# Kernel tuning notes

Measured on AMD Instinct MI355X. Metric: run time of the kernel, lower is better.

## Reference

```python
import jax, jax.numpy as jnp
import numpy as np

L = 3          # atom_decoder_depth
HEADS = 8      # spatial attention heads
T_HEADS = 8    # temporal attention heads
WQ = 32        # atoms_per_window_queries
HK = 128       # atoms_per_window_keys
EPS = 1e-5


def _ln(x, g=None, b=None):
    mu = jnp.mean(x, -1, keepdims=True)
    v = jnp.mean((x - mu) ** 2, -1, keepdims=True)
    xn = (x - mu) * jax.lax.rsqrt(v + EPS)
    if g is not None:
        xn = xn * g + b
    return xn


def _adaln(a, s, w_sc, b_sc, w_sk):
    # adaptive LN: sigmoid-scaled normed activations + conditioned skip
    sn = _ln(s)
    return jax.nn.sigmoid(sn @ w_sc + b_sc) * _ln(a) + sn @ w_sk


def setup_inputs() -> dict:
    key = jax.random.key(0)
    ks = iter(jax.random.split(key, 64))
    B0, T, N, M, D, TS = 1, 8, 1024, 4096, 256, 768
    HID = 2 * D

    def rn(shape, s=1.0):
        return jax.random.normal(next(ks), shape, jnp.float32) * s

    NW = (M + WQ - 1) // WQ
    a = rn((B0 * T, N, 2 * TS))
    q = rn((B0 * T, M, D))
    c = rn((B0 * T, M, D))
    atom_dec_bias = rn((B0, NW, WQ, HK, L * HEADS), 0.1)
    tok_idx = jnp.sort(jax.random.randint(next(ks), (B0, M), 0, N), axis=-1)
    atom_to_token = jax.nn.one_hot(tok_idx, N, dtype=jnp.float32)
    atom_pad_mask = jnp.ones((B0, M), bool)
    timestamps = jnp.sort(jax.random.uniform(next(ks), (B0, T)) * 10.0, axis=-1)
    p = 0.02
    return dict(
        a=a, q=q, c=c, atom_dec_bias=atom_dec_bias,
        atom_to_token=atom_to_token, atom_pad_mask=atom_pad_mask,
        timestamps=timestamps,
        W_a2q=rn((2 * TS, D), p),
        ada1_sw=rn((L, D, D), p), ada1_sb=rn((L, D), p), ada1_kw=rn((L, D, D), p),
        attn_wq=rn((L, D, D), p), attn_bq=rn((L, D), p),
        attn_wk=rn((L, D, D), p), attn_wv=rn((L, D, D), p),
        attn_wg=rn((L, D, D), p), attn_wo=rn((L, D, D), p),
        og_w=rn((L, D, D), p), og_b=rn((L, D), p),
        ada2_sw=rn((L, D, D), p), ada2_sb=rn((L, D), p), ada2_kw=rn((L, D, D), p),
        tr_w1=rn((L, D, HID), p), tr_w2=rn((L, D, HID), p), tr_w3=rn((L, HID, D), p),
        tr_gw=rn((L, D, D), p), tr_gb=rn((L, D), p),
        t_ln_g=jnp.ones((L, D)), t_ln_b=jnp.zeros((L, D)),
        t_wq=rn((L, D, D), p), t_wk=rn((L, D, D), p), t_wv=rn((L, D, D), p),
        t_wg=rn((L, D, D), p), t_wo=rn((L, D, D), p),
        t_decay=rn((L, T_HEADS)),
        pos_g=jnp.ones((D,)), pos_b=jnp.zeros((D,)), pos_w=rn((D, 3), p),
        T=8,
    )


def _forward(a, q, c, atom_dec_bias, atom_to_token, atom_pad_mask, timestamps,
             W_a2q, ada1_sw, ada1_sb, ada1_kw, attn_wq, attn_bq, attn_wk,
             attn_wv, attn_wg, attn_wo, og_w, og_b, ada2_sw, ada2_sb, ada2_kw,
             tr_w1, tr_w2, tr_w3, tr_gw, tr_gb, t_ln_g, t_ln_b, t_wq, t_wk,
             t_wv, t_wg, t_wo, t_decay, pos_g, pos_b, pos_w, T):
    BT, N, _ = a.shape
    B0 = BT // T
    M0, D = q.shape[1], q.shape[2]
    NW = (M0 + WQ - 1) // WQ
    M = NW * WQ
    h, dh = HEADS, D // HEADS
    th, tdh = T_HEADS, D // T_HEADS

    # token -> atom gather via one-hot matmul (atom_to_token shared across T)
    a2q = jnp.einsum('bmn,btnd->btmd', atom_to_token,
                     (a @ W_a2q).reshape(B0, T, N, D)).reshape(BT, M0, D)
    q = q + a2q

    pad = M - M0
    qf = jnp.pad(q, ((0, 0), (0, pad), (0, 0)))
    cf = jnp.pad(c, ((0, 0), (0, pad), (0, 0)))
    mask = jnp.pad(atom_pad_mask, ((0, 0), (0, pad)))  # (B0, M)

    side = (HK - WQ) // 2
    # index map: query window w attends keys [w*WQ - side, w*WQ - side + HK)
    widx = jnp.arange(NW)[:, None] * WQ + jnp.arange(HK)[None, :]

    def window_keys(x):  # (B, M, D) -> (B, NW, HK, D)
        xp = jnp.pad(x, ((0, 0), (side, side), (0, 0)))
        return xp[:, widx]

    kmask = jnp.pad(mask, ((0, 0), (side, side)))[:, widx]  # (B0, NW, HK)
    neg = jnp.where(kmask[:, None, :, None, None, :], 0.0, -1e9)

    bias = atom_dec_bias.reshape(B0, NW, WQ, HK, L, HEADS)
    inv_s = 1.0 / np.sqrt(dh).astype(np.float32)
    inv_t = 1.0 / np.sqrt(tdh).astype(np.float32)
    dt = jnp.abs(timestamps[:, :, None] - timestamps[:, None, :])  # (B0,T,T)

    for i in range(L):
        # ---- spatial windowed attention with pair bias ----
        b = _adaln(qf, cf, ada1_sw[i], ada1_sb[i], ada1_kw[i])
        qh = (b @ attn_wq[i] + attn_bq[i]).reshape(BT, NW, WQ, h, dh)
        kin = window_keys(b)                                   # (BT,NW,HK,D)
        kh = (kin @ attn_wk[i]).reshape(BT, NW, HK, h, dh)
        vh = (kin @ attn_wv[i]).reshape(BT, NW, HK, h, dh)
        logits = jnp.einsum('bnqhd,bnkhd->bnhqk', qh, kh) * inv_s
        logits = logits.reshape(B0, T, NW, h, WQ, HK)
        logits = logits + bias[:, :, :, :, i].transpose(0, 1, 4, 2, 3)[:, None] + neg
        p_attn = jax.nn.softmax(logits, axis=-1).reshape(BT, NW, h, WQ, HK)
        o = jnp.einsum('bnhqk,bnkhd->bnqhd', p_attn, vh)
        g = jax.nn.sigmoid(b @ attn_wg[i]).reshape(BT, NW, WQ, h, dh)
        o = (g * o).reshape(BT, M, D) @ attn_wo[i]
        qf = qf + jax.nn.sigmoid(cf @ og_w[i] + og_b[i]) * o
        # conditioned SwiGLU transition
        t = _adaln(qf, cf, ada2_sw[i], ada2_sb[i], ada2_kw[i])
        x = jax.nn.silu(t @ tr_w1[i]) * (t @ tr_w2[i])
        qf = qf + jax.nn.sigmoid(cf @ tr_gw[i] + tr_gb[i]) * (x @ tr_w3[i])
        # ---- temporal attention with per-head decay bias ----
        xt = qf.reshape(B0, T, M, D).transpose(0, 2, 1, 3)     # (B0,M,T,D)
        xn = _ln(xt, t_ln_g[i], t_ln_b[i])
        tq = (xn @ t_wq[i]).reshape(B0, M, T, th, tdh)
        tk = (xn @ t_wk[i]).reshape(B0, M, T, th, tdh)
        tv = (xn @ t_wv[i]).reshape(B0, M, T, th, tdh)
        tl = jnp.einsum('bmqhd,bmkhd->bmhqk', tq, tk) * inv_t
        decay = jax.nn.softplus(t_decay[i])                    # (th,)
        tl = tl - decay[None, None, :, None, None] * dt[:, None, None]
        tp = jax.nn.softmax(tl, axis=-1)
        to = jnp.einsum('bmhqk,bmkhd->bmqhd', tp, tv).reshape(B0, M, T, D)
        tg = jax.nn.sigmoid(xn @ t_wg[i])
        xt = xt + (tg * to) @ t_wo[i]
        qf = xt.transpose(0, 2, 1, 3).reshape(BT, M, D)

    q_out = qf[:, :M0]
    return _ln(q_out, pos_g, pos_b) @ pos_w  # (B*T, M0, 3)


def reference(a, q, c, atom_dec_bias, atom_to_token, atom_pad_mask, timestamps,
              W_a2q, ada1_sw, ada1_sb, ada1_kw, attn_wq, attn_bq, attn_wk,
              attn_wv, attn_wg, attn_wo, og_w, og_b, ada2_sw, ada2_sb, ada2_kw,
              tr_w1, tr_w2, tr_w3, tr_gw, tr_gb, t_ln_g, t_ln_b, t_wq, t_wk,
              t_wv, t_wg, t_wo, t_decay, pos_g, pos_b, pos_w, T):
    return _forward(a, q, c, atom_dec_bias, atom_to_token, atom_pad_mask,
                    timestamps, W_a2q, ada1_sw, ada1_sb, ada1_kw, attn_wq,
                    attn_bq, attn_wk, attn_wv, attn_wg, attn_wo, og_w, og_b,
                    ada2_sw, ada2_sb, ada2_kw, tr_w1, tr_w2, tr_w3, tr_gw,
                    tr_gb, t_ln_g, t_ln_b, t_wq, t_wk, t_wv, t_wg, t_wo,
                    t_decay, pos_g, pos_b, pos_w, T)
```

## Files before the change

kernel.cpp:

```cpp
#include <hip/hip_runtime.h>
#include <cstddef>
#include <cstdint>

#define DEVI __device__ __forceinline__

typedef __attribute__((ext_vector_type(8))) __bf16 bf16x8;
typedef __attribute__((ext_vector_type(8))) unsigned short us8;
typedef __attribute__((ext_vector_type(4))) unsigned short us4;
typedef __attribute__((ext_vector_type(4))) float f32x4;

constexpr int B0_ = 1, T_ = 8, N_ = 1024, M_ = 4096, D_ = 256;
constexpr int BT_ = 8, NW_ = 128, WQ_ = 32, HK_ = 128, SIDE_ = 48;
constexpr int R_ = BT_ * M_;
constexpr size_t Fq = 8388608;

DEVI unsigned short f2b(float f) {
  return __builtin_bit_cast(unsigned short, static_cast<__bf16>(f));
}
DEVI float b2f(unsigned short s) { return __uint_as_float(((unsigned)s) << 16); }
DEVI float sigm(float x) { return 1.0f / (1.0f + __expf(-x)); }
DEVI bf16x8 ld_bf8(const unsigned short* p) {
  return __builtin_bit_cast(bf16x8, *(const us8*)p);
}
DEVI bf16x8 pack_f8(float4 v0, float4 v1) {
  bf16x8 r;
  r[0] = (__bf16)v0.x; r[1] = (__bf16)v0.y; r[2] = (__bf16)v0.z; r[3] = (__bf16)v0.w;
  r[4] = (__bf16)v1.x; r[5] = (__bf16)v1.y; r[6] = (__bf16)v1.z; r[7] = (__bf16)v1.w;
  return r;
}
DEVI void mfma_bf16(f32x4& c, bf16x8 a, bf16x8 b) {
  c = __builtin_amdgcn_mfma_f32_16x16x32_bf16(a, b, c, 0, 0, 0);
}
DEVI void gload16(const void* g, void* l) {
  __builtin_amdgcn_global_load_lds((__attribute__((address_space(1))) void*)g,
                                   (__attribute__((address_space(3))) void*)l, 16, 0, 0);
}

struct ConvArgs {
  const float* src[64];
  int doff[64];
  int Kd[64];
  int Nd[64];
  float scale[64];
  int n;
};

__global__ __launch_bounds__(256) void conv_k(ConvArgs ca, unsigned short* __restrict__ wbf) {
  int e = blockIdx.x;
  int K = ca.Kd[e], N = ca.Nd[e];
  int nx = N >> 6, nk = K >> 6;
  int t = blockIdx.y;
  if (t >= nx * nk) return;
  int tx = t % nx, tk = t / nx;
  const float* s = ca.src[e];
  float sc = ca.scale[e];
  unsigned short* d = wbf + ca.doff[e];
  int n = tx * 64 + (threadIdx.x & 63);
  int k0 = tk * 64 + (threadIdx.x >> 6) * 16;
  for (int r = 0; r < 16; r++) {
    int k = k0 + r;
    d[(size_t)n * K + k] = f2b(s[(size_t)k * N + n] * sc);
  }
}

__global__ __launch_bounds__(256) void cvt_k(const float* __restrict__ s,
                                             unsigned short* __restrict__ d, int n8) {
  int i = blockIdx.x * 256 + threadIdx.x;
  if (i >= n8) return;
  float4 v0 = *(const float4*)(s + (size_t)i * 8);
  float4 v1 = *(const float4*)(s + (size_t)i * 8 + 4);
  *(us8*)(d + (size_t)i * 8) = __builtin_bit_cast(us8, pack_f8(v0, v1));
}

__global__ __launch_bounds__(256) void bias_prep_k(
    const float* __restrict__ bq, const float* __restrict__ sb1,
    const float* __restrict__ sb2, const float* __restrict__ ogb,
    const float* __restrict__ trb, float* __restrict__ bias) {
  int t = threadIdx.x;
  const float inv_s = 0.17677669529663687f;
  for (int i = t; i < 1024 + 3 * 2560; i += 256) bias[i] = 0.f;
  __syncthreads();
  for (int i = 0; i < 3; i++) {
    float* B = bias + 1024 + i * 2560;
    B[t]        = bq[i * 256 + t] * inv_s;
    B[1024 + t] = sb1[i * 256 + t];
    B[1536 + t] = sb2[i * 256 + t];
    B[2048 + t] = ogb[i * 256 + t];
    B[2304 + t] = trb[i * 256 + t];
  }
}

__global__ __launch_bounds__(256) void biasb_k(const float* __restrict__ adb,
                                               unsigned short* __restrict__ biasb) {
  __shared__ float ld[3072];
  int rq = blockIdx.x;
  int t = threadIdx.x;
  const float* src = adb + (size_t)rq * 3072;
  for (int i = t; i < 3072; i += 256) ld[i] = src[i];
  __syncthreads();
  int k = t & 127;
  int pk = (k & 15) * 8 + (k >> 4);
  int ak = (rq >> 5) * 32 - SIDE_ + k;
  float maskv = ((unsigned)ak < (unsigned)M_) ? 0.f : -1e9f;
  for (int lh = t >> 7; lh < 24; lh += 2)
    biasb[((size_t)lh * 4096 + rq) * 128 + pk] = f2b(ld[k * 24 + lh] + maskv);
}

__global__ __launch_bounds__(256) void tokidx_k(const float* __restrict__ a2t,
                                                int* __restrict__ idx) {
  int m = blockIdx.x * 4 + (threadIdx.x >> 6);
  int lane = threadIdx.x & 63;
  int best = -1;
  for (int j = 0; j < 16; j++) {
    int col = lane * 16 + j;
    if (a2t[(size_t)m * 1024 + col] > 0.5f) best = col;
  }
#pragma unroll
  for (int off = 1; off < 64; off <<= 1) best = max(best, __shfl_xor(best, off));
  if (lane == 0) idx[m] = best;
}

__global__ __launch_bounds__(256) void qfinitln_k(const float* __restrict__ q,
                                                  const unsigned short* __restrict__ tokf,
                                                  const int* __restrict__ idx,
                                                  float* __restrict__ qf,
                                                  unsigned short* __restrict__ lnout) {
  int wid = threadIdx.x >> 6, lane = threadIdx.x & 63;
  size_t row = (size_t)blockIdx.x * 4 + wid;
  int m = (int)(row & 4095);
  int bt = (int)(row >> 12);
  float4 qv = *(const float4*)(q + row * 256 + lane * 4);
  us4 tv = *(const us4*)(tokf + ((size_t)bt * 1024 + idx[m]) * 256 + lane * 4);
  float x[4];
  x[0] = qv.x + b2f(tv[0]); x[1] = qv.y + b2f(tv[1]);
  x[2] = qv.z + b2f(tv[2]); x[3] = qv.w + b2f(tv[3]);
  *(float4*)(qf + row * 256 + lane * 4) = make_float4(x[0], x[1], x[2], x[3]);
  float s = x[0] + x[1] + x[2] + x[3];
  float sq = x[0] * x[0] + x[1] * x[1] + x[2] * x[2] + x[3] * x[3];
#pragma unroll
  for (int o = 1; o < 64; o <<= 1) {
    s += __shfl_xor(s, o);
    sq += __shfl_xor(sq, o);
  }
  float mu = s * 0.00390625f;
  float rs = rsqrtf(sq * 0.00390625f - mu * mu + 1e-5f);
  us4 r;
#pragma unroll
  for (int j = 0; j < 4; j++) r[j] = f2b((x[j] - mu) * rs);
  *(us4*)(lnout + row * 256 + lane * 4) = r;
}

__global__ __launch_bounds__(256) void ln_k(const float* __restrict__ src,
                                            unsigned short* __restrict__ dst) {
  size_t row = (size_t)blockIdx.x * 4 + (threadIdx.x >> 6);
  int lane = threadIdx.x & 63;
  float4 v = ((const float4*)(src + row * 256))[lane];
  float s = v.x + v.y + v.z + v.w;
#pragma unroll
  for (int o = 1; o < 64; o <<= 1) s += __shfl_xor(s, o);
  float mu = s * 0.00390625f;
  float dx = v.x - mu, dy = v.y - mu, dz = v.z - mu, dw = v.w - mu;
  float qv = dx * dx + dy * dy + dz * dz + dw * dw;
#pragma unroll
  for (int o = 1; o < 64; o <<= 1) qv += __shfl_xor(qv, o);
  float rs = rsqrtf(qv * 0.00390625f + 1e-5f);
  us4 r;
  r[0] = f2b(dx * rs); r[1] = f2b(dy * rs); r[2] = f2b(dz * rs); r[3] = f2b(dw * rs);
  *(us4*)(dst + row * 256 + lane * 4) = r;
}

template <int K, int EP, int PAIR>
__global__ __launch_bounds__(256) void gemm4_k(
    const unsigned short* __restrict__ A, const unsigned short* __restrict__ Wt,
    const float* __restrict__ bias, unsigned short* __restrict__ out,
    const unsigned short* __restrict__ lnq, unsigned short* __restrict__ vtb,
    int NOUT) {
  constexpr int NT = K / 64;
  __shared__ __align__(16) unsigned short S[2][16384];
  const int tid = threadIdx.x;
  const int lane = tid & 63, w = tid >> 6;
  const int lg = lane >> 4, lr = lane & 15;
  const int wr = w >> 1, wc = w & 1;
  const size_t m_base = (size_t)blockIdx.x * 128;
  const size_t n_base = (size_t)blockIdx.y * 64;
  const int srow = w * 8 + (lane >> 3);
  const int scol = ((lane & 7) ^ (lane >> 3)) * 8;
  const unsigned short* gA = A + (m_base + srow) * K + scol;
  const unsigned short* gB = Wt + (n_base + srow) * K + scol;
  const unsigned short* gB2 = Wt + (n_base + PAIR + srow) * K + scol;
  f32x4 acc[4][2] = {};
  f32x4 acc2[4][2] = {};
  const int swz = lr & 7;

  auto stage = [&](int buf, int t) {
    unsigned short* Sb = S[buf];
    const int kk = t * 64;
#pragma unroll
    for (int j = 0; j < 4; j++)
      gload16(gA + (size_t)(j * 32) * K + kk, Sb + w * 512 + j * 2048);
#pragma unroll
    for (int j = 0; j < 2; j++)
      gload16(gB + (size_t)(j * 32) * K + kk, Sb + 8192 + w * 512 + j * 2048);
#pragma unroll
    for (int j = 0; j < 2; j++)
      gload16(gB2 + (size_t)(j * 32) * K + kk, Sb + 12288 + w * 512 + j * 2048);
  };
  auto compute = [&](int buf) {
    const unsigned short* Sb = S[buf];
#pragma unroll
    for (int ks = 0; ks < 2; ks++) {
      const int co = ((ks * 4 + lg) ^ swz) << 3;
      bf16x8 af[4], b1[2], b2[2];
#pragma unroll
      for (int i = 0; i < 4; i++)
        af[i] = ld_bf8(Sb + (wr * 64 + i * 16 + lr) * 64 + co);
#pragma unroll
      for (int i = 0; i < 2; i++) {
        b1[i] = ld_bf8(Sb + 8192 + (wc * 32 + i * 16 + lr) * 64 + co);
        b2[i] = ld_bf8(Sb + 12288 + (wc * 32 + i * 16 + lr) * 64 + co);
      }
      __builtin_amdgcn_s_setprio(1);
#pragma unroll
      for (int mi = 0; mi < 4; mi++)
#pragma unroll
        for (int ni = 0; ni < 2; ni++) {
          mfma_bf16(acc[mi][ni], af[mi], b1[ni]);
          mfma_bf16(acc2[mi][ni], af[mi], b2[ni]);
        }
      __builtin_amdgcn_s_setprio(0);
    }
  };

  stage(0, 0);
  __syncthreads();
  int cur = 0;
  for (int t = 0; t < NT - 1; t++) {
    stage(cur ^ 1, t + 1);
    compute(cur);
    __syncthreads();
    cur ^= 1;
  }
  compute(cur);
  __syncthreads();

  unsigned short* St = S[0];
  auto emit_half = [&](int cbase, bool second) {
#pragma unroll
    for (int mi = 0; mi < 4; mi++)
#pragma unroll
      for (int ni = 0; ni < 2; ni++)
#pragma unroll
        for (int r = 0; r < 4; r++) {
          int rowl = wr * 64 + mi * 16 + lg * 4 + r;
          int cl = wc * 32 + ni * 16 + lr;
          float v = (second ? acc2[mi][ni][r] : acc[mi][ni][r]) + bias[cbase + cl];
          St[rowl * 64 + (((cl >> 3) ^ (rowl & 7)) << 3) + (cl & 7)] = f2b(v);
        }
    __syncthreads();
#pragma unroll
    for (int p = 0; p < 4; p++) {
      int rowl = p * 32 + (tid >> 3);
      int chunk = tid & 7;
      us8 v = *(const us8*)(St + rowl * 64 + ((chunk ^ (rowl & 7)) << 3));
      *(us8*)(out + (m_base + rowl) * NOUT + cbase + chunk * 8) = v;
    }
    __syncthreads();
  };

  if constexpr (EP == 1) {
    emit_half((int)n_base, false);
    emit_half((int)n_base + PAIR, true);
  } else if constexpr (EP == 6) {
    emit_half((int)n_base, false);
    if ((int)n_base < 256) {
      const int bt = (int)(m_base >> 12);
      const int m0 = (int)(m_base & 4095);
#pragma unroll
      for (int mi = 0; mi < 4; mi++)
#pragma unroll
        for (int ni = 0; ni < 2; ni++) {
          int cl = wc * 32 + ni * 16 + lr;
          int rowb = wr * 64 + mi * 16 + lg * 4;
          us4 val;
#pragma unroll
          for (int r = 0; r < 4; r++)
            val[r] = f2b(acc2[mi][ni][r] + bias[(int)n_base + cl + 512]);
          *(us4*)(St + cl * 128 + (((rowb >> 3) ^ (cl & 7)) << 3) + (rowb & 7)) = val;
        }
      __syncthreads();
#pragma unroll
      for (int p = 0; p < 4; p++) {
        int cl = tid >> 2;
        int rc = (tid & 3) + p * 4;
        us8 v = *(const us8*)(St + cl * 128 + ((rc ^ (cl & 7)) << 3));
        *(us8*)(vtb + ((size_t)bt * 256 + n_base + cl) * 4096 + m0 + rc * 8) = v;
      }
    } else {
      emit_half((int)n_base + 512, true);
    }
  } else {
#pragma unroll
    for (int mi = 0; mi < 4; mi++)
#pragma unroll
      for (int ni = 0; ni < 2; ni++)
#pragma unroll
        for (int r = 0; r < 4; r++) {
          int rowl = wr * 64 + mi * 16 + lg * 4 + r;
          int cl = wc * 32 + ni * 16 + lr;
          size_t grow = m_base + rowl;
          int gcol = (int)n_base + cl;
          float v = acc[mi][ni][r] + bias[gcol];
          float v2 = acc2[mi][ni][r] + bias[gcol + PAIR];
          unsigned short res;
          if constexpr (EP == 4) {
            res = f2b(sigm(v) * b2f(lnq[grow * 256 + gcol]) + v2);
          } else {
            res = f2b(v * sigm(v) * v2);
          }
          St[rowl * 64 + (((cl >> 3) ^ (rowl & 7)) << 3) + (cl & 7)] = res;
        }
    __syncthreads();
#pragma unroll
    for (int p = 0; p < 4; p++) {
      int rowl = p * 32 + (tid >> 3);
      int chunk = tid & 7;
      us8 v = *(const us8*)(St + rowl * 64 + ((chunk ^ (rowl & 7)) << 3));
      *(us8*)(out + (m_base + rowl) * NOUT + n_base + chunk * 8) = v;
    }
  }
}

template <int K, bool GATED>
__global__ __launch_bounds__(512) void gemmln_k(
    const unsigned short* __restrict__ A, const unsigned short* __restrict__ Wt,
    float* __restrict__ qf, const unsigned short* __restrict__ gate, int goff,
    unsigned short* __restrict__ lnout, const float* __restrict__ lng,
    const float* __restrict__ lnb) {
  constexpr int NT = K / 64;
  __shared__ __align__(16) unsigned short S[2][20480];
  const int tid = threadIdx.x;
  const int lane = tid & 63, w = tid >> 6;
  const int lg = lane >> 4, lr = lane & 15;
  const size_t m_base = (size_t)blockIdx.x * 64;
  const int srow = lane >> 3;
  const int scol = ((lane & 7) ^ srow) * 8;
  const unsigned short* gA = A + (m_base + w * 8 + srow) * K + scol;
  const unsigned short* gB = Wt + (w * 32 + srow) * K + scol;
  f32x4 acc[4][2] = {};
  const int swz = lr & 7;

  auto stage = [&](int buf, int t) {
    unsigned short* Sb = S[buf];
    const int kk = t * 64;
    gload16(gA + kk, Sb + w * 512);
#pragma unroll
    for (int j = 0; j < 4; j++)
      gload16(gB + (size_t)(j * 8) * K + kk, Sb + 4096 + w * 2048 + j * 512);
  };
  auto compute = [&](int buf) {
    const unsigned short* Sb = S[buf];
#pragma unroll
    for (int ks = 0; ks < 2; ks++) {
      const int co = ((ks * 4 + lg) ^ swz) << 3;
      bf16x8 af[4], bf1[2];
#pragma unroll
      for (int i = 0; i < 4; i++) af[i] = ld_bf8(Sb + (i * 16 + lr) * 64 + co);
#pragma unroll
      for (int i = 0; i < 2; i++)
        bf1[i] = ld_bf8(Sb + 4096 + (w * 32 + i * 16 + lr) * 64 + co);
      __builtin_amdgcn_s_setprio(1);
#pragma unroll
      for (int mi = 0; mi < 4; mi++)
#pragma unroll
        for (int ni = 0; ni < 2; ni++) mfma_bf16(acc[mi][ni], af[mi], bf1[ni]);
      __builtin_amdgcn_s_setprio(0);
    }
  };

  stage(0, 0);
  __syncthreads();
  int cur = 0;
  for (int t = 0; t < NT - 1; t++) {
    stage(cur ^ 1, t + 1);
    compute(cur);
    __syncthreads();
    cur ^= 1;
  }
  compute(cur);
  __syncthreads();

  unsigned short* St = S[0];
#pragma unroll
  for (int mi = 0; mi < 4; mi++)
#pragma unroll
    for (int ni = 0; ni < 2; ni++)
#pragma unroll
      for (int r = 0; r < 4; r++) {
        int rowl = mi * 16 + lg * 4 + r;
        int col = w * 32 + ni * 16 + lr;
        size_t grow = m_base + rowl;
        float v = acc[mi][ni][r];
        if constexpr (GATED) v *= sigm(b2f(gate[grow * 512 + goff + col]));
        float nq = qf[grow * 256 + col] + v;
        qf[grow * 256 + col] = nq;
        St[rowl * 256 + (((col >> 3) ^ (rowl & 7)) << 3) + (col & 7)] = f2b(nq);
      }
  __syncthreads();
  float gv[4], bv[4];
  if (lng) {
#pragma unroll
    for (int j = 0; j < 4; j++) {
      gv[j] = lng[lane * 4 + j];
      bv[j] = lnb[lane * 4 + j];
    }
  }
  const int rchunk = lane >> 1;
  const int rsub = (lane & 1) << 2;
  for (int rr = 0; rr < 8; rr++) {
    int rowl = w * 8 + rr;
    us4 vv = *(const us4*)(St + rowl * 256 + ((rchunk ^ (rowl & 7)) << 3) + rsub);
    float x[4];
#pragma unroll
    for (int j = 0; j < 4; j++) x[j] = b2f(vv[j]);
    float s = x[0] + x[1] + x[2] + x[3];
    float sq = x[0] * x[0] + x[1] * x[1] + x[2] * x[2] + x[3] * x[3];
#pragma unroll
    for (int o = 1; o < 64; o <<= 1) {
      s += __shfl_xor(s, o);
      sq += __shfl_xor(sq, o);
    }
    float mu = s * 0.00390625f;
    float rs = rsqrtf(sq * 0.00390625f - mu * mu + 1e-5f);
    us4 r;
#pragma unroll
    for (int j = 0; j < 4; j++) {
      float y = (x[j] - mu) * rs;
      if (lng) y = y * gv[j] + bv[j];
      r[j] = f2b(y);
    }
    *(us4*)(lnout + (m_base + rowl) * 256 + lane * 4) = r;
  }
}

__global__ __launch_bounds__(256) void attn_k(const unsigned short* __restrict__ big1,
                                              const unsigned short* __restrict__ vtbuf,
                                              const unsigned short* __restrict__ biasb,
                                              unsigned short* __restrict__ o, int layer) {
  __shared__ __align__(16) unsigned short pl_s[4][32 * 128];
  const int bid = blockIdx.x;
  const int nid = (bid & 7) * 256 + (bid >> 3);
  const int w = nid & 127, bt = (nid >> 7) & 7, hg = nid >> 10;
  const int tid = threadIdx.x, wid = tid >> 6, lane = tid & 63;
  const int lg = lane >> 4, lr = lane & 15;
  const int h = hg * 4 + wid;
  unsigned short* pl = pl_s[wid];
  const size_t base = (size_t)bt * M_;

  bf16x8 aq[2];
#pragma unroll
  for (int mi = 0; mi < 2; mi++)
    aq[mi] = ld_bf8(big1 + (base + w * 32 + mi * 16 + lr) * 1024 + h * 32 + lg * 8);
  f32x4 lac[2][8] = {};
#pragma unroll
  for (int ni = 0; ni < 8; ni++) {
    int kidx = ni * 16 + lr;
    int ak = w * 32 - SIDE_ + kidx;
    int akc = ak < 0 ? 0 : (ak > M_ - 1 ? M_ - 1 : ak);
    bf16x8 bk = ld_bf8(big1 + (base + akc) * 1024 + 256 + h * 32 + lg * 8);
    __builtin_amdgcn_s_setprio(1);
    mfma_bf16(lac[0][ni], aq[0], bk);
    mfma_bf16(lac[1][ni], aq[1], bk);
    __builtin_amdgcn_s_setprio(0);
  }
  const unsigned short* bb0 =
      biasb + (((size_t)(layer * 8 + h)) * 4096 + w * 32) * 128 + lr * 8;
  float invs[2][4];
#pragma unroll
  for (int mi = 0; mi < 2; mi++)
#pragma unroll
    for (int r = 0; r < 4; r++) {
      int qrow = mi * 16 + lg * 4 + r;
      us8 bb = *(const us8*)(bb0 + (size_t)qrow * 128);
      float lv[8];
      float mx = -3e38f;
#pragma unroll
      for (int ni = 0; ni < 8; ni++) {
        float x = lac[mi][ni][r] + b2f(bb[ni]);
        lv[ni] = x;
        mx = fmaxf(mx, x);
      }
#pragma unroll
      for (int off = 1; off < 16; off <<= 1) mx = fmaxf(mx, __shfl_xor(mx, off));
      float sum = 0.f;
#pragma unroll
      for (int ni = 0; ni < 8; ni++) {
        float e = __expf(lv[ni] - mx);
        lv[ni] = e;
        sum += e;
      }
#pragma unroll
      for (int off = 1; off < 16; off <<= 1) sum += __shfl_xor(sum, off);
      invs[mi][r] = 1.f / sum;
      int sw = (qrow & 7) << 3;
#pragma unroll
      for (int ni = 0; ni < 8; ni++)
        pl[qrow * 128 + ((ni * 16 + lr) ^ sw)] = f2b(lv[ni]);
    }
  const unsigned short* vrow0 = vtbuf + ((size_t)bt * 256 + h * 32 + lr) * 4096;
  const unsigned short* vrow1 = vrow0 + (size_t)16 * 4096;
  f32x4 oc[2][2] = {};
#pragma unroll
  for (int ks = 0; ks < 4; ks++) {
    int kcol = w * 32 - SIDE_ + ks * 32 + lg * 8;
    kcol = kcol < 0 ? 0 : (kcol > M_ - 8 ? M_ - 8 : kcol);
    bf16x8 bv0 = ld_bf8(vrow0 + kcol);
    bf16x8 bv1 = ld_bf8(vrow1 + kcol);
    int kswz = (ks * 32 + lg * 8) ^ ((lr & 7) << 3);
    bf16x8 ap0 = ld_bf8(pl + lr * 128 + kswz);
    bf16x8 ap1 = ld_bf8(pl + (16 + lr) * 128 + kswz);
    __builtin_amdgcn_s_setprio(1);
    mfma_bf16(oc[0][0], ap0, bv0);
    mfma_bf16(oc[0][1], ap0, bv1);
    mfma_bf16(oc[1][0], ap1, bv0);
    mfma_bf16(oc[1][1], ap1, bv1);
    __builtin_amdgcn_s_setprio(0);
  }
#pragma unroll
  for (int mi = 0; mi < 2; mi++)
#pragma unroll
    for (int nd = 0; nd < 2; nd++)
#pragma unroll
      for (int r = 0; r < 4; r++) {
        int qrow = mi * 16 + lg * 4 + r;
        int d = nd * 16 + lr;
        size_t rowi = base + w * 32 + qrow;
        float gv = sigm(b2f(big1[rowi * 1024 + 768 + h * 32 + d]));
        o[rowi * 256 + h * 32 + d] = f2b(oc[mi][nd][r] * invs[mi][r] * gv);
      }
}

__global__ __launch_bounds__(256) void tattn_k(const unsigned short* __restrict__ big1,
                                               const float* __restrict__ ts,
                                               const float* __restrict__ tdec,
                                               unsigned short* __restrict__ o, int layer) {
  __shared__ __align__(16) unsigned short lds[4][8 * 768];
  int wid = threadIdx.x >> 6, lane = threadIdx.x & 63;
  int m = blockIdx.x * 4 + wid;
  unsigned short* Lp = lds[wid];
  for (int it = 0; it < 12; it++) {
    int u = it * 64 + lane;
    int t = u / 96, pos = (u % 96) * 8;
    *(uint4*)(Lp + t * 768 + pos) =
        *(const uint4*)(big1 + ((size_t)(t * M_ + m)) * 1024 + pos);
  }
  __syncthreads();
  int th = lane >> 3, qt = lane & 7;
  float decay = log1pf(__expf(tdec[layer * 8 + th]));
  float tsq = ts[qt];
  const float inv_t = 0.17677669529663687f;
  float tqv[32];
#pragma unroll
  for (int d = 0; d < 32; d++) tqv[d] = b2f(Lp[qt * 768 + th * 32 + d]);
  float lv[8];
  float mx = -3e38f;
#pragma unroll
  for (int kt = 0; kt < 8; kt++) {
    float dot = 0.f;
#pragma unroll
    for (int d = 0; d < 32; d++) dot += tqv[d] * b2f(Lp[kt * 768 + 256 + th * 32 + d]);
    float x = dot * inv_t - decay * fabsf(tsq - ts[kt]);
    lv[kt] = x;
    mx = fmaxf(mx, x);
  }
  float s = 0.f;
#pragma unroll
  for (int kt = 0; kt < 8; kt++) {
    float e = __expf(lv[kt] - mx);
    lv[kt] = e;
    s += e;
  }
  float inv = 1.f / s;
  float tov[32];
#pragma unroll
  for (int d = 0; d < 32; d++) tov[d] = 0.f;
#pragma unroll
  for (int kt = 0; kt < 8; kt++) {
    float p = lv[kt] * inv;
#pragma unroll
    for (int d = 0; d < 32; d++) tov[d] += p * b2f(Lp[kt * 768 + 512 + th * 32 + d]);
  }
  size_t orow = (size_t)qt * M_ + m;
#pragma unroll
  for (int d = 0; d < 32; d++) {
    float tg = sigm(b2f(big1[orow * 1024 + 768 + th * 32 + d]));
    o[orow * 256 + th * 32 + d] = f2b(tov[d] * tg);
  }
}

__global__ __launch_bounds__(256) void final_k(const float* __restrict__ qf,
                                               const float* __restrict__ pg,
                                               const float* __restrict__ pb,
                                               const float* __restrict__ pw,
                                               float* __restrict__ out) {
  size_t row = (size_t)blockIdx.x * 4 + (threadIdx.x >> 6);
  int lane = threadIdx.x & 63;
  float4 v = ((const float4*)(qf + row * 256))[lane];
  float s = v.x + v.y + v.z + v.w;
#pragma unroll
  for (int o = 1; o < 64; o <<= 1) s += __shfl_xor(s, o);
  float mu = s * 0.00390625f;
  float dx = v.x - mu, dy = v.y - mu, dz = v.z - mu, dw = v.w - mu;
  float qv = dx * dx + dy * dy + dz * dz + dw * dw;
#pragma unroll
  for (int o = 1; o < 64; o <<= 1) qv += __shfl_xor(qv, o);
  float rs = rsqrtf(qv * 0.00390625f + 1e-5f);
  int d = lane * 4;
  float xn[4];
  xn[0] = dx * rs * pg[d] + pb[d];
  xn[1] = dy * rs * pg[d + 1] + pb[d + 1];
  xn[2] = dz * rs * pg[d + 2] + pb[d + 2];
  xn[3] = dw * rs * pg[d + 3] + pb[d + 3];
  float p0 = 0.f, p1 = 0.f, p2 = 0.f;
#pragma unroll
  for (int dd = 0; dd < 4; dd++) {
    const float* wr = pw + (size_t)(d + dd) * 3;
    p0 += xn[dd] * wr[0];
    p1 += xn[dd] * wr[1];
    p2 += xn[dd] * wr[2];
  }
#pragma unroll
  for (int o = 1; o < 64; o <<= 1) {
    p0 += __shfl_xor(p0, o);
    p1 += __shfl_xor(p1, o);
    p2 += __shfl_xor(p2, o);
  }
  if (lane == 0) {
    out[row * 3 + 0] = p0;
    out[row * 3 + 1] = p1;
    out[row * 3 + 2] = p2;
  }
}

extern "C" void kernel_launch(void* const* d_in, const int* in_sizes, int n_in,
                              void* d_out, int out_size, void* d_ws, size_t ws_size,
                              hipStream_t stream) {
  const float* a       = (const float*)d_in[0];
  const float* q_in    = (const float*)d_in[1];
  const float* c_in    = (const float*)d_in[2];
  const float* adb     = (const float*)d_in[3];
  const float* a2t     = (const float*)d_in[4];
  const float* ts      = (const float*)d_in[6];
  const float* W_a2q   = (const float*)d_in[7];
  const float* ada1_sw = (const float*)d_in[8];
  const float* ada1_sb = (const float*)d_in[9];
  const float* ada1_kw = (const float*)d_in[10];
  const float* attn_wq = (const float*)d_in[11];
  const float* attn_bq = (const float*)d_in[12];
  const float* attn_wk = (const float*)d_in[13];
  const float* attn_wv = (const float*)d_in[14];
  const float* attn_wg = (const float*)d_in[15];
  const float* attn_wo = (const float*)d_in[16];
  const float* og_w    = (const float*)d_in[17];
  const float* og_b    = (const float*)d_in[18];
  const float* ada2_sw = (const float*)d_in[19];
  const float* ada2_sb = (const float*)d_in[20];
  const float* ada2_kw = (const float*)d_in[21];
  const float* tr_w1   = (const float*)d_in[22];
  const float* tr_w2   = (const float*)d_in[23];
  const float* tr_w3   = (const float*)d_in[24];
  const float* tr_gw   = (const float*)d_in[25];
  const float* tr_gb   = (const float*)d_in[26];
  const float* t_ln_g  = (const float*)d_in[27];
  const float* t_ln_b  = (const float*)d_in[28];
  const float* t_wq    = (const float*)d_in[29];
  const float* t_wk    = (const float*)d_in[30];
  const float* t_wv    = (const float*)d_in[31];
  const float* t_wg    = (const float*)d_in[32];
  const float* t_wo    = (const float*)d_in[33];
  const float* t_dec   = (const float*)d_in[34];
  const float* pos_g   = (const float*)d_in[35];
  const float* pos_b   = (const float*)d_in[36];
  const float* pos_w   = (const float*)d_in[37];

  char* base = (char*)d_ws;
  size_t off = 0;
  auto alloc = [&](size_t bytes) {
    void* p = base + off;
    off += (bytes + 255) & ~(size_t)255;
    return p;
  };
  float* qf            = (float*)alloc(Fq * 4);
  unsigned short* lncb = (unsigned short*)alloc(Fq * 2);
  unsigned short* lnqb = (unsigned short*)alloc(Fq * 2);
  unsigned short* obuf = (unsigned short*)alloc(Fq * 2);
  unsigned short* big1 = (unsigned short*)alloc(Fq * 8);
  unsigned short* bbuf = (unsigned short*)alloc(Fq * 2);
  unsigned short* cbf  = (unsigned short*)alloc(Fq * 2);
  unsigned short* vtbuf= (unsigned short*)alloc(Fq * 2);
  unsigned short* biasb= (unsigned short*)alloc((size_t)24 * 4096 * 128 * 2);
  unsigned short* wbf  = (unsigned short*)alloc((size_t)4718592 * 2);
  float* biasr         = (float*)alloc(8704 * 4);
  int* tokidx          = (int*)alloc(4096 * 4);

  unsigned short* xbuf  = big1;
  unsigned short* ggate = big1 + (size_t)R_ * 512;
  unsigned short* abf   = big1;
  unsigned short* tokf  = big1 + 2 * Fq;

  ConvArgs ca;
  int ne = 0;
  auto add = [&](const float* s, size_t doff, int K, int N, float sc) {
    ca.src[ne] = s; ca.doff[ne] = (int)doff; ca.Kd[ne] = K; ca.Nd[ne] = N;
    ca.scale[ne] = sc; ne++;
  };
  const float inv_s = 0.17677669529663687f;
  constexpr size_t LW = 1441792;
  for (int i = 0; i < 3; i++) {
    size_t LB = (size_t)i * LW;
    add(ada1_sw + i * 65536, LB + 0, 256, 256, 1.f);
    add(ada1_kw + i * 65536, LB + 65536, 256, 256, 1.f);
    add(attn_wq + i * 65536, LB + 131072, 256, 256, inv_s);
    add(attn_wk + i * 65536, LB + 196608, 256, 256, 1.f);
    add(attn_wv + i * 65536, LB + 262144, 256, 256, 1.f);
    add(attn_wg + i * 65536, LB + 327680, 256, 256, 1.f);
    add(attn_wo + i * 65536, LB + 393216, 256, 256, 1.f);
    add(og_w + i * 65536, LB + 458752, 256, 256, 1.f);
    add(tr_gw + i * 65536, LB + 524288, 256, 256, 1.f);
    add(ada2_sw + i * 65536, LB + 589824, 256, 256, 1.f);
    add(ada2_kw + i * 65536, LB + 655360, 256, 256, 1.f);
    add(tr_w1 + i * 131072, LB + 720896, 256, 512, 1.f);
    add(tr_w2 + i * 131072, LB + 851968, 256, 512, 1.f);
    add(tr_w3 + i * 131072, LB + 983040, 512, 256, 1.f);
    add(t_wq + i * 65536, LB + 1114112, 256, 256, 1.f);
    add(t_wk + i * 65536, LB + 1179648, 256, 256, 1.f);
    add(t_wv + i * 65536, LB + 1245184, 256, 256, 1.f);
    add(t_wg + i * 65536, LB + 1310720, 256, 256, 1.f);
    add(t_wo + i * 65536, LB + 1376256, 256, 256, 1.f);
  }
  add(W_a2q, 3 * LW, 1536, 256, 1.f);
  ca.n = ne;

  conv_k<<<dim3(ne, 96), 256, 0, stream>>>(ca, wbf);
  bias_prep_k<<<1, 256, 0, stream>>>(attn_bq, ada1_sb, ada2_sb, og_b, tr_gb, biasr);
  tokidx_k<<<1024, 256, 0, stream>>>(a2t, tokidx);
  biasb_k<<<4096, 256, 0, stream>>>(adb, biasb);
  cvt_k<<<6144, 256, 0, stream>>>(a, abf, 1572864);
  cvt_k<<<4096, 256, 0, stream>>>(c_in, cbf, 1048576);
  gemm4_k<1536, 1, 128><<<dim3(64, 2), 256, 0, stream>>>(
      abf, wbf + 3 * LW, biasr, tokf, nullptr, nullptr, 256);
  qfinitln_k<<<8192, 256, 0, stream>>>(q_in, tokf, tokidx, qf, lnqb);
  ln_k<<<8192, 256, 0, stream>>>(c_in, lncb);

  for (int i = 0; i < 3; i++) {
    size_t LB = (size_t)i * LW;
    const float* b_attn = biasr + 1024 + (size_t)i * 2560;
    const float* b_ada1 = b_attn + 1024;
    const float* b_ada2 = b_attn + 1536;
    const float* b_ogtr = b_attn + 2048;

    gemm4_k<256, 4, 256><<<dim3(256, 4), 256, 0, stream>>>(
        lncb, wbf + LB, b_ada1, bbuf, lnqb, nullptr, 256);
    gemm4_k<256, 6, 512><<<dim3(256, 8), 256, 0, stream>>>(
        bbuf, wbf + LB + 131072, b_attn, big1, nullptr, vtbuf, 1024);
    attn_k<<<2048, 256, 0, stream>>>(big1, vtbuf, biasb, obuf, i);
    gemm4_k<256, 1, 256><<<dim3(256, 4), 256, 0, stream>>>(
        cbf, wbf + LB + 458752, b_ogtr, ggate, nullptr, nullptr, 512);
    gemmln_k<256, true><<<512, 512, 0, stream>>>(
        obuf, wbf + LB + 393216, qf, ggate, 0, lnqb, nullptr, nullptr);
    gemm4_k<256, 4, 256><<<dim3(256, 4), 256, 0, stream>>>(
        lncb, wbf + LB + 589824, b_ada2, bbuf, lnqb, nullptr, 256);
    gemm4_k<256, 5, 512><<<dim3(256, 8), 256, 0, stream>>>(
        bbuf, wbf + LB + 720896, biasr, xbuf, nullptr, nullptr, 512);
    gemmln_k<512, true><<<512, 512, 0, stream>>>(
        xbuf, wbf + LB + 983040, qf, ggate, 256, lnqb,
        t_ln_g + (size_t)i * 256, t_ln_b + (size_t)i * 256);
    gemm4_k<256, 1, 512><<<dim3(256, 8), 256, 0, stream>>>(
        lnqb, wbf + LB + 1114112, biasr, big1, nullptr, nullptr, 1024);
    tattn_k<<<1024, 256, 0, stream>>>(big1, ts, t_dec, obuf, i);
    gemmln_k<256, false><<<512, 512, 0, stream>>>(
        obuf, wbf + LB + 1376256, qf, nullptr, 0, lnqb, nullptr, nullptr);
  }
  final_k<<<8192, 256, 0, stream>>>(qf, pos_g, pos_b, pos_w, (float*)d_out);
}
```

Before: 1.123 ms.

## Fuse temporal QKVG projection with temporal attention and retile gemmln staging

Adds a kernel that computes the temporal Q/K/V/gate projection per head into shared memory and runs the 8-timestep attention directly from there. This drops the separate projection GEMM and attention kernels and avoids writing and re-reading the large intermediate QKVG buffer through global memory. The LayerNorm-fused GEMM is also retiled to a K-step of 32, with half the waves loading A and half loading B, which cuts shared memory use. The tradeoffs are a grid of only 256 blocks that loop serially over heads, and an attention phase in which only half the threads are active.

```diff
diff --git a/kernel.cpp b/kernel.cpp
--- a/kernel.cpp
+++ b/kernel.cpp
@@ -330,51 +330,182 @@
   }
 }
 
+__global__ __launch_bounds__(256) void tfuse_k(
+    const unsigned short* __restrict__ A, const unsigned short* __restrict__ Wb,
+    const float* __restrict__ ts, const float* __restrict__ tdec,
+    unsigned short* __restrict__ o, int layer) {
+  __shared__ __align__(16) unsigned short S[2 * 8192];
+  const int tid = threadIdx.x;
+  const int lane = tid & 63, w = tid >> 6;
+  const int lg = lane >> 4, lr = lane & 15;
+  const int m0 = blockIdx.x * 16;
+  const int srow = lane >> 2;
+  const int scol = ((lane & 3) ^ ((lane >> 3) & 3)) * 8;
+  const int co = (lg ^ ((lr >> 1) & 3)) << 3;
+  const unsigned short* gA0 = A + ((size_t)(2 * w) * M_ + m0 + srow) * 256 + scol;
+  const unsigned short* gA1 = A + ((size_t)(2 * w + 1) * M_ + m0 + srow) * 256 + scol;
+  const unsigned short* gBp = Wb + (size_t)w * 65536 + (size_t)srow * 256 + scol;
+  const float inv_t = 0.17677669529663687f;
+
+  for (int h = 0; h < 8; h++) {
+    const unsigned short* gB = gBp + (size_t)h * 32 * 256;
+    f32x4 acc[2][8] = {};
+    auto stage = [&](int buf, int t) {
+      unsigned short* Sb = S + buf * 8192;
+      const int kk = t * 32;
+      gload16(gA0 + kk, Sb + w * 1024);
+      gload16(gA1 + kk, Sb + w * 1024 + 512);
+      gload16(gB + kk, Sb + 4096 + w * 1024);
+      gload16(gB + 16 * 256 + kk, Sb + 4096 + w * 1024 + 512);
+    };
+    auto compute = [&](int buf) {
+      const unsigned short* Sb = S + buf * 8192;
+      bf16x8 af[2], bfr[8];
+#pragma unroll
+      for (int i = 0; i < 2; i++)
+        af[i] = ld_bf8(Sb + (w * 32 + i * 16 + lr) * 32 + co);
+#pragma unroll
+      for (int i = 0; i < 8; i++)
+        bfr[i] = ld_bf8(Sb + 4096 + (i * 16 + lr) * 32 + co);
+      __builtin_amdgcn_s_setprio(1);
+#pragma unroll
+      for (int mi = 0; mi < 2; mi++)
+#pragma unroll
+        for (int ni = 0; ni < 8; ni++) mfma_bf16(acc[mi][ni], af[mi], bfr[ni]);
+      __builtin_amdgcn_s_setprio(0);
+    };
+    stage(0, 0);
+    __syncthreads();
+    int cur = 0;
+    for (int t = 0; t < 7; t++) {
+      stage(cur ^ 1, t + 1);
+      compute(cur);
+      __syncthreads();
+      cur ^= 1;
+    }
+    compute(cur);
+    __syncthreads();
+#pragma unroll
+    for (int mi = 0; mi < 2; mi++)
+#pragma unroll
+      for (int ni = 0; ni < 8; ni++)
+#pragma unroll
+        for (int r = 0; r < 4; r++) {
+          int row = w * 32 + mi * 16 + lg * 4 + r;
+          int c = ni * 16 + lr;
+          S[row * 128 + (((c >> 3) ^ (row & 7)) << 3) + (c & 7)] = f2b(acc[mi][ni][r]);
+        }
+    __syncthreads();
+    if (tid < 128) {
+      const int a = tid & 15, qt = tid >> 4;
+      const float decay = log1pf(__expf(tdec[layer * 8 + h]));
+      const float tsq = ts[qt];
+      const int rq = qt * 16 + a, swq = rq & 7;
+      float qv[32];
+#pragma unroll
+      for (int j = 0; j < 4; j++) {
+        us8 u = *(const us8*)(S + rq * 128 + ((j ^ swq) << 3));
+#pragma unroll
+        for (int e = 0; e < 8; e++) qv[j * 8 + e] = b2f(u[e]);
+      }
+      float lv[8], mx = -3e38f;
+#pragma unroll
+      for (int kt = 0; kt < 8; kt++) {
+        int rk = kt * 16 + a, swk = rk & 7;
+        float dot = 0.f;
+#pragma unroll
+        for (int j = 0; j < 4; j++) {
+          us8 u = *(const us8*)(S + rk * 128 + (((4 + j) ^ swk) << 3));
+#pragma unroll
+          for (int e = 0; e < 8; e++) dot += qv[j * 8 + e] * b2f(u[e]);
+        }
+        float x = dot * inv_t - decay * fabsf(tsq - ts[kt]);
+        lv[kt] = x;
+        mx = fmaxf(mx, x);
+      }
+      float sum = 0.f;
+#pragma unroll
+      for (int kt = 0; kt < 8; kt++) {
+        float e = __expf(lv[kt] - mx);
+        lv[kt] = e;
+        sum += e;
+      }
+      float inv = 1.f / sum;
+      float ov[32];
+#pragma unroll
+      for (int d = 0; d < 32; d++) ov[d] = 0.f;
+#pragma unroll
+      for (int kt = 0; kt < 8; kt++) {
+        int rk = kt * 16 + a, swk = rk & 7;
+        float p = lv[kt];
+#pragma unroll
+        for (int j = 0; j < 4; j++) {
+          us8 u = *(const us8*)(S + rk * 128 + (((8 + j) ^ swk) << 3));
+#pragma unroll
+          for (int e = 0; e < 8; e++) ov[j * 8 + e] += p * b2f(u[e]);
+        }
+      }
+      unsigned short* dst = o + ((size_t)qt * M_ + m0 + a) * 256 + h * 32;
+#pragma unroll
+      for (int j = 0; j < 4; j++) {
+        us8 gvv = *(const us8*)(S + rq * 128 + (((12 + j) ^ swq) << 3));
+        us8 r;
+#pragma unroll
+        for (int e = 0; e < 8; e++)
+          r[e] = f2b(ov[j * 8 + e] * inv * sigm(b2f(gvv[e])));
+        *(us8*)(dst + j * 8) = r;
+      }
+    }
+    __syncthreads();
+  }
+}
+
 template <int K, bool GATED>
 __global__ __launch_bounds__(512) void gemmln_k(
     const unsigned short* __restrict__ A, const unsigned short* __restrict__ Wt,
     float* __restrict__ qf, const unsigned short* __restrict__ gate, int goff,
     unsigned short* __restrict__ lnout, const float* __restrict__ lng,
     const float* __restrict__ lnb) {
-  constexpr int NT = K / 64;
-  __shared__ __align__(16) unsigned short S[2][20480];
+  constexpr int NT = K / 32;
+  __shared__ __align__(16) unsigned short S[2 * 10240];
   const int tid = threadIdx.x;
   const int lane = tid & 63, w = tid >> 6;
   const int lg = lane >> 4, lr = lane & 15;
   const size_t m_base = (size_t)blockIdx.x * 64;
-  const int srow = lane >> 3;
-  const int scol = ((lane & 7) ^ srow) * 8;
-  const unsigned short* gA = A + (m_base + w * 8 + srow) * K + scol;
-  const unsigned short* gB = Wt + (w * 32 + srow) * K + scol;
+  const int srow = lane >> 2;
+  const int scol = ((lane & 3) ^ ((lane >> 3) & 3)) * 8;
+  const unsigned short* gA =
+      (w < 4) ? A + (m_base + w * 16 + srow) * K + scol : nullptr;
+  const unsigned short* gB =
+      (w >= 4) ? Wt + ((size_t)((w - 4) * 16 + srow)) * K + scol : nullptr;
   f32x4 acc[4][2] = {};
-  const int swz = lr & 7;
+  const int co = (lg ^ ((lr >> 1) & 3)) << 3;
 
   auto stage = [&](int buf, int t) {
-    unsigned short* Sb = S[buf];
-    const int kk = t * 64;
-    gload16(gA + kk, Sb + w * 512);
-#pragma unroll
-    for (int j = 0; j < 4; j++)
-      gload16(gB + (size_t)(j * 8) * K + kk, Sb + 4096 + w * 2048 + j * 512);
+    unsigned short* Sb = S + buf * 10240;
+    const int kk = t * 32;
+    if (w < 4) {
+      gload16(gA + kk, Sb + w * 512);
+    } else {
+#pragma unroll
+      for (int j = 0; j < 4; j++)
+        gload16(gB + (size_t)(j * 64) * K + kk, Sb + 2048 + (w - 4) * 512 + j * 2048);
+    }
   };
   auto compute = [&](int buf) {
-    const unsigned short* Sb = S[buf];
-#pragma unroll
-    for (int ks = 0; ks < 2; ks++) {
-      const int co = ((ks * 4 + lg) ^ swz) << 3;
-      bf16x8 af[4], bf1[2];
-#pragma unroll
-      for (int i = 0; i < 4; i++) af[i] = ld_bf8(Sb + (i * 16 + lr) * 64 + co);
-#pragma unroll
-      for (int i = 0; i < 2; i++)
-        bf1[i] = ld_bf8(Sb + 4096 + (w * 32 + i * 16 + lr) * 64 + co);
-      __builtin_amdgcn_s_setprio(1);
-#pragma unroll
-      for (int mi = 0; mi < 4; mi++)
-#pragma unroll
-        for (int ni = 0; ni < 2; ni++) mfma_bf16(acc[mi][ni], af[mi], bf1[ni]);
-      __builtin_amdgcn_s_setprio(0);
-    }
+    const unsigned short* Sb = S + buf * 10240;
+    bf16x8 af[4], bf1[2];
+#pragma unroll
+    for (int i = 0; i < 4; i++) af[i] = ld_bf8(Sb + (i * 16 + lr) * 32 + co);
+#pragma unroll
+    for (int i = 0; i < 2; i++)
+      bf1[i] = ld_bf8(Sb + 2048 + (w * 32 + i * 16 + lr) * 32 + co);
+    __builtin_amdgcn_s_setprio(1);
+#pragma unroll
+    for (int mi = 0; mi < 4; mi++)
+#pragma unroll
+      for (int ni = 0; ni < 2; ni++) mfma_bf16(acc[mi][ni], af[mi], bf1[ni]);
+    __builtin_amdgcn_s_setprio(0);
   };
 
   stage(0, 0);
@@ -389,7 +520,7 @@
   compute(cur);
   __syncthreads();
 
-  unsigned short* St = S[0];
+  unsigned short* St = S;
 #pragma unroll
   for (int mi = 0; mi < 4; mi++)
 #pragma unroll
@@ -537,64 +668,6 @@
         float gv = sigm(b2f(big1[rowi * 1024 + 768 + h * 32 + d]));
         o[rowi * 256 + h * 32 + d] = f2b(oc[mi][nd][r] * invs[mi][r] * gv);
       }
-}
-
-__global__ __launch_bounds__(256) void tattn_k(const unsigned short* __restrict__ big1,
-                                               const float* __restrict__ ts,
-                                               const float* __restrict__ tdec,
-                                               unsigned short* __restrict__ o, int layer) {
-  __shared__ __align__(16) unsigned short lds[4][8 * 768];
-  int wid = threadIdx.x >> 6, lane = threadIdx.x & 63;
-  int m = blockIdx.x * 4 + wid;
-  unsigned short* Lp = lds[wid];
-  for (int it = 0; it < 12; it++) {
-    int u = it * 64 + lane;
-    int t = u / 96, pos = (u % 96) * 8;
-    *(uint4*)(Lp + t * 768 + pos) =
-        *(const uint4*)(big1 + ((size_t)(t * M_ + m)) * 1024 + pos);
-  }
-  __syncthreads();
-  int th = lane >> 3, qt = lane & 7;
-  float decay = log1pf(__expf(tdec[layer * 8 + th]));
-  float tsq = ts[qt];
-  const float inv_t = 0.17677669529663687f;
-  float tqv[32];
-#pragma unroll
-  for (int d = 0; d < 32; d++) tqv[d] = b2f(Lp[qt * 768 + th * 32 + d]);
-  float lv[8];
-  float mx = -3e38f;
-#pragma unroll
-  for (int kt = 0; kt < 8; kt++) {
-    float dot = 0.f;
-#pragma unroll
-    for (int d = 0; d < 32; d++) dot += tqv[d] * b2f(Lp[kt * 768 + 256 + th * 32 + d]);
-    float x = dot * inv_t - decay * fabsf(tsq - ts[kt]);
-    lv[kt] = x;
-    mx = fmaxf(mx, x);
-  }
-  float s = 0.f;
-#pragma unroll
-  for (int kt = 0; kt < 8; kt++) {
-    float e = __expf(lv[kt] - mx);
-    lv[kt] = e;
-    s += e;
-  }
-  float inv = 1.f / s;
-  float tov[32];
-#pragma unroll
-  for (int d = 0; d < 32; d++) tov[d] = 0.f;
-#pragma unroll
-  for (int kt = 0; kt < 8; kt++) {
-    float p = lv[kt] * inv;
-#pragma unroll
-    for (int d = 0; d < 32; d++) tov[d] += p * b2f(Lp[kt * 768 + 512 + th * 32 + d]);
-  }
-  size_t orow = (size_t)qt * M_ + m;
-#pragma unroll
-  for (int d = 0; d < 32; d++) {
-    float tg = sigm(b2f(big1[orow * 1024 + 768 + th * 32 + d]));
-    o[orow * 256 + th * 32 + d] = f2b(tov[d] * tg);
-  }
 }
 
 __global__ __launch_bounds__(256) void final_k(const float* __restrict__ qf,
@@ -774,9 +847,7 @@
     gemmln_k<512, true><<<512, 512, 0, stream>>>(
         xbuf, wbf + LB + 983040, qf, ggate, 256, lnqb,
         t_ln_g + (size_t)i * 256, t_ln_b + (size_t)i * 256);
-    gemm4_k<256, 1, 512><<<dim3(256, 8), 256, 0, stream>>>(
-        lnqb, wbf + LB + 1114112, biasr, big1, nullptr, nullptr, 1024);
-    tattn_k<<<1024, 256, 0, stream>>>(big1, ts, t_dec, obuf, i);
+    tfuse_k<<<256, 256, 0, stream>>>(lnqb, wbf + LB + 1114112, ts, t_dec, obuf, i);
     gemmln_k<256, false><<<512, 512, 0, stream>>>(
         obuf, wbf + LB + 1376256, qf, nullptr, 0, lnqb, nullptr, nullptr);
   }
```

New measurement: 1.179 ms. 4.9% more time.
